# Optimization experiments

Hardware: AMD Instinct MI355X
Metric: run time of the kernel (lower is better)

## Reference

```python
import jax, jax.numpy as jnp
import numpy as np

HEADS = 16
ROPE_BASE = 10000.0


def _rope(x, cos, sin):
    # x: [B, H, L, hd]; rotate_half = [-x2, x1]
    x1, x2 = jnp.split(x, 2, axis=-1)
    rot = jnp.concatenate((-x2, x1), axis=-1)
    return x * cos + rot * sin


def setup_inputs() -> dict:
    key = jax.random.key(0)
    ks = jax.random.split(key, 8)
    B, L, D = 2, 2048, 1024
    s = 0.02
    inp = {
        "Q": jax.random.normal(ks[0], (B, L, D), jnp.float32),
        "K": jax.random.normal(ks[1], (B, L, D), jnp.float32),
        "V": jax.random.normal(ks[2], (B, L, D), jnp.float32),
        # Linear weights stored as [in, out] (transpose of torch's [out, in])
        "Wq": jax.random.normal(ks[3], (D, D), jnp.float32) * s,
        "Wk": jax.random.normal(ks[4], (D, D), jnp.float32) * s,
        "Wv": jax.random.normal(ks[5], (D, D), jnp.float32) * s,
        "Wo": jax.random.normal(ks[6], (D, D), jnp.float32) * s,
        "bq": jnp.zeros((D,), jnp.float32),
        "bk": jnp.zeros((D,), jnp.float32),
        "bv": jnp.zeros((D,), jnp.float32),
        "bo": jnp.zeros((D,), jnp.float32),
        # causal mask, 0 = masked, broadcast to [B,1,L,L]
        "mask": jnp.broadcast_to(jnp.tril(jnp.ones((L, L), jnp.int32))[None, None], (B, 1, L, L)),
    }
    return inp


def reference(Q, K, V, Wq, Wk, Wv, Wo, bq, bk, bv, bo, mask):
    B, L, D = Q.shape
    H = HEADS
    hd = D // H

    def proj(x, W, b):
        # [B,L,D] -> [B,H,L,hd]
        return (x @ W + b).reshape(B, -1, H, hd).transpose(0, 2, 1, 3)

    q = proj(Q, Wq, bq)
    k = proj(K, Wk, bk)
    v = proj(V, Wv, bv)

    # RoPE tables (deterministic constants)
    inv_freq = 1.0 / (ROPE_BASE ** (jnp.arange(0, hd, 2, dtype=jnp.float32) / hd))
    t = jnp.arange(L, dtype=jnp.float32)
    freqs = jnp.outer(t, inv_freq)              # [L, hd/2]
    emb = jnp.concatenate((freqs, freqs), -1)   # [L, hd]
    cos = jnp.cos(emb)[None, None]              # [1,1,L,hd]
    sin = jnp.sin(emb)[None, None]
    q = _rope(q, cos, sin)
    k = _rope(k, cos, sin)

    scale = jnp.sqrt(jnp.asarray(hd, q.dtype))
    scores = jnp.einsum('bhqd,bhkd->bhqk', q, k) / scale
    scores = jnp.where(mask == 0, jnp.asarray(-1e9, scores.dtype), scores)
    attn = jax.nn.softmax(scores, axis=-1)
    out = jnp.einsum('bhqk,bhkd->bhqd', attn, v)
    out = out.transpose(0, 2, 1, 3).reshape(B, L, D)
    return out @ Wo + bo
```

## Files before the change

kernel.cpp:

```cpp
#include <hip/hip_runtime.h>

typedef __attribute__((ext_vector_type(8))) short short8;
typedef __attribute__((ext_vector_type(4))) float f32x4;
typedef unsigned short u16;
typedef unsigned int u32;

#define MFMA_BF16(a, b, c) __builtin_amdgcn_mfma_f32_16x16x32_bf16((a), (b), (c), 0, 0, 0)

constexpr int D = 1024;
constexpr int L = 2048;
constexpr int NHEAD = 16;
constexpr int HD = 64;
constexpr float QLAMBDA = 0.125f * 1.44269504088896340736f;

__device__ __forceinline__ u16 f2bf(float f) {
  unsigned u = __builtin_bit_cast(unsigned, f);
  u = (u + 0x7fffu + ((u >> 16) & 1u)) >> 16;
  return (u16)u;
}

__device__ __forceinline__ short8 cvt8(f32x4 lo, f32x4 hi) {
  short8 r;
  r[0] = (short)f2bf(lo[0]); r[1] = (short)f2bf(lo[1]);
  r[2] = (short)f2bf(lo[2]); r[3] = (short)f2bf(lo[3]);
  r[4] = (short)f2bf(hi[0]); r[5] = (short)f2bf(hi[1]);
  r[6] = (short)f2bf(hi[2]); r[7] = (short)f2bf(hi[3]);
  return r;
}

__device__ __forceinline__ void gload16(const u16* src, u16* dst) {
  __builtin_amdgcn_global_load_lds(
      (const __attribute__((address_space(1))) u32*)(src),
      (__attribute__((address_space(3))) u32*)(dst), 16, 0, 0);
}

__global__ __launch_bounds__(256) void wt_trans_kernel(const float* W0, const float* W1,
                                                       const float* W2, const float* W3,
                                                       u16* out) {
  const float* W = blockIdx.z == 0 ? W0 : blockIdx.z == 1 ? W1 : blockIdx.z == 2 ? W2 : W3;
  u16* o = out + (size_t)blockIdx.z * D * D;
  __shared__ float t[32][33];
  int x = threadIdx.x & 31, y = threadIdx.x >> 5;
  int k0 = blockIdx.x * 32, n0 = blockIdx.y * 32;
#pragma unroll
  for (int i = 0; i < 4; i++) {
    int ky = y * 4 + i;
    t[ky][x] = W[(size_t)(k0 + ky) * D + n0 + x];
  }
  __syncthreads();
#pragma unroll
  for (int i = 0; i < 4; i++) {
    int ny = y * 4 + i;
    o[(size_t)(n0 + ny) * D + k0 + x] = f2bf(t[x][ny]);
  }
}

__global__ __launch_bounds__(256) void rope_tab_kernel(float* ct, float* st) {
  int t = blockIdx.x * 256 + threadIdx.x;
  int i = t & 31, pos = t >> 5;
  float invf = powf(10000.0f, -(float)i / 32.0f);
  float ang = (float)pos * invf;
  ct[t] = cosf(ang);
  st[t] = sinf(ang);
}

__global__ __launch_bounds__(256) void cvt_x_kernel(const float* Q, const float* K,
                                                    const float* V, u16* xb) {
  const float* src = blockIdx.y == 0 ? Q : blockIdx.y == 1 ? K : V;
  u16* dst = xb + (size_t)blockIdx.y * 4096 * D;
  int t = blockIdx.x * 256 + threadIdx.x;
  const float* p = src + (size_t)t * 8;
  f32x4 lo = *(const f32x4*)p;
  f32x4 hi = *(const f32x4*)(p + 4);
  *(short8*)(dst + (size_t)t * 8) = cvt8(lo, hi);
}


__global__ __launch_bounds__(256, 3) void proj_gemm_staged(
    const u16* xb, const u16* wT,
    const float* bq, const float* bk, const float* bv,
    const float* ct, const float* st,
    u16* qo, u16* ko, u16* vT) {
  int i = blockIdx.x;
  int swz = (i & 7) * 96 + (i >> 3);
  int z = swz >> 8;
  int bx = swz & 7;
  int by = (swz >> 3) & 31;

  const u16* A = xb + (size_t)z * 4096 * D;
  const u16* W = wT + (size_t)z * D * D;
  const float* bias = z == 0 ? bq : z == 1 ? bk : bv;

  int w = threadIdx.x >> 6, lane = threadIdx.x & 63;
  int r = lane & 15, c = lane >> 4;
  int wr = w >> 1, wc = w & 1;
  int m0 = by * 128 + wr * 64;
  int n0 = bx * 128 + wc * 64;

  __shared__ __align__(16) u16 lsA[2][4096];
  __shared__ __align__(16) u16 lsB[2][4096];

  const u16* aSrc[2];
  const u16* bSrc[2];
  int dstOff[2];
#pragma unroll
  for (int i2 = 0; i2 < 2; i2++) {
    int q0 = i2 * 256 + w * 64;
    int qq = q0 + lane;
    int t = qq >> 2;
    int gch = (qq & 3) ^ ((t >> 1) & 3);
    aSrc[i2] = A + (size_t)(by * 128 + t) * D + gch * 8;
    bSrc[i2] = W + (size_t)(bx * 128 + t) * D + gch * 8;
    dstOff[i2] = q0 * 8;
  }

  int aOff[4], bOff[4];
#pragma unroll
  for (int mi = 0; mi < 4; mi++) {
    int rowA = wr * 64 + mi * 16 + r;
    aOff[mi] = rowA * 32 + ((c ^ ((rowA >> 1) & 3)) << 3);
    int rowB = wc * 64 + mi * 16 + r;
    bOff[mi] = rowB * 32 + ((c ^ ((rowB >> 1) & 3)) << 3);
  }

  f32x4 acc[4][4];
#pragma unroll
  for (int mi = 0; mi < 4; mi++)
#pragma unroll
    for (int ni = 0; ni < 4; ni++) acc[mi][ni] = f32x4{0.f, 0.f, 0.f, 0.f};

#pragma unroll
  for (int i2 = 0; i2 < 2; i2++) {
    gload16(aSrc[i2], &lsA[0][dstOff[i2]]);
    gload16(bSrc[i2], &lsB[0][dstOff[i2]]);
  }

  auto compute = [&](const u16* pa, const u16* pb) {
    short8 af[4], bf[4];
#pragma unroll
    for (int mi = 0; mi < 4; mi++) af[mi] = *(const short8*)(pa + aOff[mi]);
#pragma unroll
    for (int ni = 0; ni < 4; ni++) bf[ni] = *(const short8*)(pb + bOff[ni]);
#pragma unroll
    for (int mi = 0; mi < 4; mi++)
#pragma unroll
      for (int ni = 0; ni < 4; ni++)
        acc[mi][ni] = MFMA_BF16(af[mi], bf[ni], acc[mi][ni]);
  };

  for (int kt = 0; kt < 31; kt++) {
    int cur = kt & 1;
    __syncthreads();
#pragma unroll
    for (int i2 = 0; i2 < 2; i2++) {
      gload16(aSrc[i2] + (kt + 1) * 32, &lsA[cur ^ 1][dstOff[i2]]);
      gload16(bSrc[i2] + (kt + 1) * 32, &lsB[cur ^ 1][dstOff[i2]]);
    }
    compute(lsA[cur], lsB[cur]);
  }
  __syncthreads();
  compute(lsA[1], lsB[1]);

  int h = n0 >> 6;
#pragma unroll
  for (int mi = 0; mi < 4; mi++) {
#pragma unroll
    for (int j = 0; j < 4; j++) {
      int grow = m0 + mi * 16 + c * 4 + j;
      int b = grow >> 11, ll = grow & 2047;
      if (z < 2) {
        u16* o = (z == 0) ? qo : ko;
        float lam = (z == 0) ? QLAMBDA : 1.0f;
        size_t dst = ((size_t)(b * NHEAD + h) * L + ll) * HD;
#pragma unroll
        for (int ni = 0; ni < 2; ni++) {
          int d = ni * 16 + r;
          float x1 = acc[mi][ni][j] + bias[n0 + d];
          float x2 = acc[mi][ni + 2][j] + bias[n0 + 32 + d];
          float cs = ct[ll * 32 + d], sn = st[ll * 32 + d];
          o[dst + d]      = f2bf((x1 * cs - x2 * sn) * lam);
          o[dst + d + 32] = f2bf((x2 * cs + x1 * sn) * lam);
        }
      } else {
#pragma unroll
        for (int ni = 0; ni < 4; ni++) {
          int d = ni * 16 + r;
          float val = acc[mi][ni][j] + bias[n0 + d];
          vT[((size_t)(b * NHEAD + h) * HD + d) * L + ll] = f2bf(val);
        }
      }
    }
  }
}

__global__ __launch_bounds__(256) void proj_gemm_f32(
    const float* Qf, const float* Kf, const float* Vf, const u16* wT,
    const float* bq, const float* bk, const float* bv,
    const float* ct, const float* st,
    u16* qo, u16* ko, u16* vT) {
  int i = blockIdx.x;
  int swz = (i & 7) * 96 + (i >> 3);
  int z = swz >> 8;
  int bx = swz & 7;
  int by = (swz >> 3) & 31;

  const u16* W = wT + (size_t)z * D * D;
  const float* bias = z == 0 ? bq : z == 1 ? bk : bv;

  int w = threadIdx.x >> 6, lane = threadIdx.x & 63;
  int r = lane & 15, c = lane >> 4;
  int wr = w >> 1, wc = w & 1;
  int m0 = by * 128 + wr * 64;
  int n0 = bx * 128 + wc * 64;

  const float* Af = z == 0 ? Qf : z == 1 ? Kf : Vf;
  const float* a0f = Af + (size_t)(m0 + r) * D + c * 8;
  const u16* b0 = W + (size_t)(n0 + r) * D + c * 8;

  f32x4 acc[4][4];
#pragma unroll
  for (int mi = 0; mi < 4; mi++)
#pragma unroll
    for (int ni = 0; ni < 4; ni++) acc[mi][ni] = f32x4{0.f, 0.f, 0.f, 0.f};

  for (int kk = 0; kk < D; kk += 32) {
    short8 af[4], bf[4];
#pragma unroll
    for (int mi = 0; mi < 4; mi++) {
      const float* ap = a0f + (size_t)mi * 16 * D;
      af[mi] = cvt8(*(const f32x4*)ap, *(const f32x4*)(ap + 4));
    }
#pragma unroll
    for (int ni = 0; ni < 4; ni++) bf[ni] = *(const short8*)(b0 + (size_t)ni * 16 * D);
#pragma unroll
    for (int mi = 0; mi < 4; mi++)
#pragma unroll
      for (int ni = 0; ni < 4; ni++)
        acc[mi][ni] = MFMA_BF16(af[mi], bf[ni], acc[mi][ni]);
    a0f += 32;
    b0 += 32;
  }

  int h = n0 >> 6;
#pragma unroll
  for (int mi = 0; mi < 4; mi++) {
#pragma unroll
    for (int j = 0; j < 4; j++) {
      int grow = m0 + mi * 16 + c * 4 + j;
      int b = grow >> 11, ll = grow & 2047;
      if (z < 2) {
        u16* o = (z == 0) ? qo : ko;
        float lam = (z == 0) ? QLAMBDA : 1.0f;
        size_t dst = ((size_t)(b * NHEAD + h) * L + ll) * HD;
#pragma unroll
        for (int ni = 0; ni < 2; ni++) {
          int d = ni * 16 + r;
          float x1 = acc[mi][ni][j] + bias[n0 + d];
          float x2 = acc[mi][ni + 2][j] + bias[n0 + 32 + d];
          float cs = ct[ll * 32 + d], sn = st[ll * 32 + d];
          o[dst + d]      = f2bf((x1 * cs - x2 * sn) * lam);
          o[dst + d + 32] = f2bf((x2 * cs + x1 * sn) * lam);
        }
      } else {
#pragma unroll
        for (int ni = 0; ni < 4; ni++) {
          int d = ni * 16 + r;
          float val = acc[mi][ni][j] + bias[n0 + d];
          vT[((size_t)(b * NHEAD + h) * HD + d) * L + ll] = f2bf(val);
        }
      }
    }
  }
}

__global__ __launch_bounds__(256) void attn_kernel(const u16* qg, const u16* kg,
                                                   const u16* vg, u16* O) {
  int i = blockIdx.x;
  int xcd = i & 7, j = i >> 3;
  int bh = xcd * 4 + (j & 3);
  int a = j >> 2;
  int qtA = a, qtB = 31 - a;

  int w = threadIdx.x >> 6, lane = threadIdx.x & 63;
  int r = lane & 15, c = lane >> 4;
  int qbA = qtA * 64 + w * 16;
  int qbB = qtB * 64 + w * 16;

  const u16* qp = qg + (size_t)bh * L * HD;
  const u16* kp = kg + (size_t)bh * L * HD;
  const u16* vp = vg + (size_t)bh * HD * L;

  __shared__ __align__(16) u16 kls[2][4096];
  __shared__ __align__(16) u16 vls[2][4096];
  __shared__ __align__(16) u16 plds[4][16][64];

  short8 aqA0 = *(const short8*)(qp + (size_t)(qbA + r) * HD + c * 8);
  short8 aqA1 = *(const short8*)(qp + (size_t)(qbA + r) * HD + 32 + c * 8);
  short8 aqB0 = *(const short8*)(qp + (size_t)(qbB + r) * HD + c * 8);
  short8 aqB1 = *(const short8*)(qp + (size_t)(qbB + r) * HD + 32 + c * 8);

  const short one_bf = (short)0x3F80;
  short8 ones = {one_bf, one_bf, one_bf, one_bf, one_bf, one_bf, one_bf, one_bf};

  f32x4 oA[4], oB[4];
  f32x4 sacA = f32x4{0.f, 0.f, 0.f, 0.f};
  f32x4 sacB = f32x4{0.f, 0.f, 0.f, 0.f};
#pragma unroll
  for (int n = 0; n < 4; n++) {
    oA[n] = f32x4{0.f, 0.f, 0.f, 0.f};
    oB[n] = f32x4{0.f, 0.f, 0.f, 0.f};
  }

  int nkt = qtB + 1;

#pragma unroll
  for (int rd = 0; rd < 2; rd++) {
    int q0 = (rd * 4 + w) << 6;
    int qq = q0 + lane;
    int row = qq >> 3;
    int gch = (qq & 7) ^ (row & 7);
    gload16(kp + (size_t)row * HD + gch * 8, &kls[0][q0 * 8]);
    gload16(vp + (size_t)row * L + gch * 8, &vls[0][q0 * 8]);
  }

  for (int kt = 0; kt < nkt; kt++) {
    int cur = kt & 1;
    __syncthreads();
    if (kt + 1 < nkt) {
      int kb2 = (kt + 1) * 64;
      const u16* kp2 = kp + (size_t)kb2 * HD;
      const u16* vp2 = vp + kb2;
#pragma unroll
      for (int rd = 0; rd < 2; rd++) {
        int q0 = (rd * 4 + w) << 6;
        int qq = q0 + lane;
        int row = qq >> 3;
        int gch = (qq & 7) ^ (row & 7);
        gload16(kp2 + (size_t)row * HD + gch * 8, &kls[cur ^ 1][q0 * 8]);
        gload16(vp2 + (size_t)row * L + gch * 8, &vls[cur ^ 1][q0 * 8]);
      }
    }
    const u16* kb_ = kls[cur];
    const u16* vb_ = vls[cur];
    int kbase = kt * 64;

    auto do_tile = [&](const short8& qf0, const short8& qf1, f32x4* o, f32x4& sac,
                       int qb, bool edge) {
      f32x4 S[4];
#pragma unroll
      for (int ks = 0; ks < 4; ks++) {
        int row = ks * 16 + r;
        short8 kf0 = *(const short8*)(kb_ + row * 64 + ((c ^ (row & 7)) << 3));
        short8 kf1 = *(const short8*)(kb_ + row * 64 + (((4 + c) ^ (row & 7)) << 3));
        S[ks] = f32x4{0.f, 0.f, 0.f, 0.f};
        S[ks] = MFMA_BF16(qf0, kf0, S[ks]);
        S[ks] = MFMA_BF16(qf1, kf1, S[ks]);
      }
#pragma unroll
      for (int j4 = 0; j4 < 4; j4++) {
        float p0 = exp2f(S[0][j4]);
        float p1 = exp2f(S[1][j4]);
        float p2 = exp2f(S[2][j4]);
        float p3 = exp2f(S[3][j4]);
        if (edge) {
          int qrow = qb + c * 4 + j4;
          if (kbase + r > qrow) p0 = 0.f;
          if (kbase + 16 + r > qrow) p1 = 0.f;
          if (kbase + 32 + r > qrow) p2 = 0.f;
          if (kbase + 48 + r > qrow) p3 = 0.f;
        }
        int prow = c * 4 + j4, xr = (prow & 7) << 3;
        plds[w][prow][(r) ^ xr]      = f2bf(p0);
        plds[w][prow][(16 + r) ^ xr] = f2bf(p1);
        plds[w][prow][(32 + r) ^ xr] = f2bf(p2);
        plds[w][prow][(48 + r) ^ xr] = f2bf(p3);
      }
      int xrr = (r & 7) << 3;
      short8 pa0 = *(const short8*)&plds[w][r][(c * 8) ^ xrr];
      short8 pa1 = *(const short8*)&plds[w][r][(32 + c * 8) ^ xrr];
      sac = MFMA_BF16(pa0, ones, sac);
      sac = MFMA_BF16(pa1, ones, sac);
#pragma unroll
      for (int n = 0; n < 4; n++) {
        int row = n * 16 + r;
        short8 vf0 = *(const short8*)(vb_ + row * 64 + ((c ^ (row & 7)) << 3));
        short8 vf1 = *(const short8*)(vb_ + row * 64 + (((4 + c) ^ (row & 7)) << 3));
        o[n] = MFMA_BF16(pa0, vf0, o[n]);
        o[n] = MFMA_BF16(pa1, vf1, o[n]);
      }
    };

    do_tile(aqB0, aqB1, oB, sacB, qbB, kt == nkt - 1);
    if (kt <= qtA) do_tile(aqA0, aqA1, oA, sacA, qbA, kt == qtA);
  }

  int b = bh >> 4, h = bh & 15;
#pragma unroll
  for (int j4 = 0; j4 < 4; j4++) {
    int qrowA = qbA + c * 4 + j4;
    int qrowB = qbB + c * 4 + j4;
    float invA = 1.0f / sacA[j4];
    float invB = 1.0f / sacB[j4];
#pragma unroll
    for (int n = 0; n < 4; n++) {
      O[((size_t)(b * L + qrowA)) * D + h * HD + n * 16 + r] = f2bf(oA[n][j4] * invA);
      O[((size_t)(b * L + qrowB)) * D + h * HD + n * 16 + r] = f2bf(oB[n][j4] * invB);
    }
  }
}

__global__ __launch_bounds__(256, 3) void oproj_gemm_staged(const u16* Ag, const u16* wT,
                                                            const float* bias, float* out) {
  int i = blockIdx.x;
  int swz = (i & 7) * 32 + (i >> 3);
  int bx = swz & 7, by = swz >> 3;

  int w = threadIdx.x >> 6, lane = threadIdx.x & 63;
  int r = lane & 15, c = lane >> 4;
  int wr = w >> 1, wc = w & 1;
  int m0 = by * 128 + wr * 64;
  int n0 = bx * 128 + wc * 64;

  __shared__ __align__(16) u16 lsA[2][4096];
  __shared__ __align__(16) u16 lsB[2][4096];

  const u16* aSrc[2];
  const u16* bSrc[2];
  int dstOff[2];
#pragma unroll
  for (int i2 = 0; i2 < 2; i2++) {
    int q0 = i2 * 256 + w * 64;
    int qq = q0 + lane;
    int t = qq >> 2;
    int gch = (qq & 3) ^ ((t >> 1) & 3);
    aSrc[i2] = Ag + (size_t)(by * 128 + t) * D + gch * 8;
    bSrc[i2] = wT + (size_t)(bx * 128 + t) * D + gch * 8;
    dstOff[i2] = q0 * 8;
  }

  int aOff[4], bOff[4];
#pragma unroll
  for (int mi = 0; mi < 4; mi++) {
    int rowA = wr * 64 + mi * 16 + r;
    aOff[mi] = rowA * 32 + ((c ^ ((rowA >> 1) & 3)) << 3);
    int rowB = wc * 64 + mi * 16 + r;
    bOff[mi] = rowB * 32 + ((c ^ ((rowB >> 1) & 3)) << 3);
  }

  f32x4 acc[4][4];
#pragma unroll
  for (int mi = 0; mi < 4; mi++)
#pragma unroll
    for (int ni = 0; ni < 4; ni++) acc[mi][ni] = f32x4{0.f, 0.f, 0.f, 0.f};

#pragma unroll
  for (int i2 = 0; i2 < 2; i2++) {
    gload16(aSrc[i2], &lsA[0][dstOff[i2]]);
    gload16(bSrc[i2], &lsB[0][dstOff[i2]]);
  }

  auto compute = [&](const u16* pa, const u16* pb) {
    short8 af[4], bf[4];
#pragma unroll
    for (int mi = 0; mi < 4; mi++) af[mi] = *(const short8*)(pa + aOff[mi]);
#pragma unroll
    for (int ni = 0; ni < 4; ni++) bf[ni] = *(const short8*)(pb + bOff[ni]);
#pragma unroll
    for (int mi = 0; mi < 4; mi++)
#pragma unroll
      for (int ni = 0; ni < 4; ni++)
        acc[mi][ni] = MFMA_BF16(af[mi], bf[ni], acc[mi][ni]);
  };

  for (int kt = 0; kt < 31; kt++) {
    int cur = kt & 1;
    __syncthreads();
#pragma unroll
    for (int i2 = 0; i2 < 2; i2++) {
      gload16(aSrc[i2] + (kt + 1) * 32, &lsA[cur ^ 1][dstOff[i2]]);
      gload16(bSrc[i2] + (kt + 1) * 32, &lsB[cur ^ 1][dstOff[i2]]);
    }
    compute(lsA[cur], lsB[cur]);
  }
  __syncthreads();
  compute(lsA[1], lsB[1]);

#pragma unroll
  for (int mi = 0; mi < 4; mi++)
#pragma unroll
    for (int j = 0; j < 4; j++) {
      int grow = m0 + mi * 16 + c * 4 + j;
#pragma unroll
      for (int ni = 0; ni < 4; ni++) {
        int gcol = n0 + ni * 16 + r;
        out[(size_t)grow * D + gcol] = acc[mi][ni][j] + bias[gcol];
      }
    }
}

extern "C" void kernel_launch(void* const* d_in, const int* in_sizes, int n_in,
                              void* d_out, int out_size, void* d_ws, size_t ws_size,
                              hipStream_t stream) {
  const float* Q = (const float*)d_in[0];
  const float* K = (const float*)d_in[1];
  const float* V = (const float*)d_in[2];
  const float* Wq = (const float*)d_in[3];
  const float* Wk = (const float*)d_in[4];
  const float* Wv = (const float*)d_in[5];
  const float* Wo = (const float*)d_in[6];
  const float* bq = (const float*)d_in[7];
  const float* bk = (const float*)d_in[8];
  const float* bv = (const float*)d_in[9];
  const float* bo = (const float*)d_in[10];
  float* out = (float*)d_out;

  char* ws = (char*)d_ws;
  u16* wT = (u16*)(ws);
  u16* woT = wT + (size_t)3 * 1024 * 1024;
  float* ct = (float*)(ws + 8388608);
  float* st = (float*)(ws + 8650752);
  u16* qbuf = (u16*)(ws + 8912896);
  u16* kbuf = (u16*)(ws + 17301504);
  u16* vbuf = (u16*)(ws + 25690112);
  u16* obuf = (u16*)(ws + 34078720);
  u16* xb = (u16*)(ws + 42467328);

  wt_trans_kernel<<<dim3(32, 32, 4), 256, 0, stream>>>(Wq, Wk, Wv, Wo, wT);
  rope_tab_kernel<<<dim3(256), 256, 0, stream>>>(ct, st);

  if (ws_size >= (size_t)67633152) {
    cvt_x_kernel<<<dim3(2048, 3), 256, 0, stream>>>(Q, K, V, xb);
    proj_gemm_staged<<<dim3(768), 256, 0, stream>>>(xb, wT, bq, bk, bv, ct, st,
                                                    qbuf, kbuf, vbuf);
  } else {
    proj_gemm_f32<<<dim3(768), 256, 0, stream>>>(Q, K, V, wT, bq, bk, bv, ct, st,
                                                 qbuf, kbuf, vbuf);
  }
  attn_kernel<<<dim3(512), 256, 0, stream>>>(qbuf, kbuf, vbuf, obuf);
  oproj_gemm_staged<<<dim3(256), 256, 0, stream>>>(obuf, woT, bo, out);
}
```

Baseline: 264.9 us.

## Merge prep kernels, use hardware bf16 convert, halve oproj tile height

Folds the weight transpose, RoPE table and input conversion kernels into one launch so fewer kernels are dispatched. Replaces the software round-to-nearest bf16 conversion with the hardware v_cvt_pk_bf16_f32 instruction in the projection epilogues and the attention kernel. Shrinks the output-projection tile from 128x128 to 64x128 and doubles its grid to 512 blocks, which spreads the work over more CUs but loads more weight data per output.

```diff
diff --git a/kernel.cpp b/kernel.cpp
--- a/kernel.cpp
+++ b/kernel.cpp
@@ -17,6 +17,12 @@
   unsigned u = __builtin_bit_cast(unsigned, f);
   u = (u + 0x7fffu + ((u >> 16) & 1u)) >> 16;
   return (u16)u;
+}
+
+__device__ __forceinline__ u16 cvt1(float f) {
+  unsigned o;
+  asm("v_cvt_pk_bf16_f32 %0, %1, %1" : "=v"(o) : "v"(f));
+  return (u16)o;
 }
 
 __device__ __forceinline__ short8 cvt8(f32x4 lo, f32x4 hi) {
@@ -34,45 +40,48 @@
       (__attribute__((address_space(3))) u32*)(dst), 16, 0, 0);
 }
 
-__global__ __launch_bounds__(256) void wt_trans_kernel(const float* W0, const float* W1,
-                                                       const float* W2, const float* W3,
-                                                       u16* out) {
-  const float* W = blockIdx.z == 0 ? W0 : blockIdx.z == 1 ? W1 : blockIdx.z == 2 ? W2 : W3;
-  u16* o = out + (size_t)blockIdx.z * D * D;
-  __shared__ float t[32][33];
-  int x = threadIdx.x & 31, y = threadIdx.x >> 5;
-  int k0 = blockIdx.x * 32, n0 = blockIdx.y * 32;
-#pragma unroll
-  for (int i = 0; i < 4; i++) {
-    int ky = y * 4 + i;
-    t[ky][x] = W[(size_t)(k0 + ky) * D + n0 + x];
-  }
-  __syncthreads();
-#pragma unroll
-  for (int i = 0; i < 4; i++) {
-    int ny = y * 4 + i;
-    o[(size_t)(n0 + ny) * D + k0 + x] = f2bf(t[x][ny]);
-  }
-}
-
-__global__ __launch_bounds__(256) void rope_tab_kernel(float* ct, float* st) {
-  int t = blockIdx.x * 256 + threadIdx.x;
-  int i = t & 31, pos = t >> 5;
-  float invf = powf(10000.0f, -(float)i / 32.0f);
-  float ang = (float)pos * invf;
-  ct[t] = cosf(ang);
-  st[t] = sinf(ang);
-}
-
-__global__ __launch_bounds__(256) void cvt_x_kernel(const float* Q, const float* K,
-                                                    const float* V, u16* xb) {
-  const float* src = blockIdx.y == 0 ? Q : blockIdx.y == 1 ? K : V;
-  u16* dst = xb + (size_t)blockIdx.y * 4096 * D;
-  int t = blockIdx.x * 256 + threadIdx.x;
-  const float* p = src + (size_t)t * 8;
-  f32x4 lo = *(const f32x4*)p;
-  f32x4 hi = *(const f32x4*)(p + 4);
-  *(short8*)(dst + (size_t)t * 8) = cvt8(lo, hi);
+template <bool DO_CVT>
+__global__ __launch_bounds__(256) void prep_kernel(
+    const float* W0, const float* W1, const float* W2, const float* W3, u16* wTout,
+    float* ct, float* st,
+    const float* Q, const float* K, const float* V, u16* xb) {
+  int i = blockIdx.x;
+  if (i < 4096) {
+    int z = i >> 10, bx = i & 31, by = (i >> 5) & 31;
+    const float* W = z == 0 ? W0 : z == 1 ? W1 : z == 2 ? W2 : W3;
+    u16* o = wTout + (size_t)z * D * D;
+    __shared__ float t[32][33];
+    int x = threadIdx.x & 31, y = threadIdx.x >> 5;
+    int k0 = bx * 32, n0 = by * 32;
+#pragma unroll
+    for (int q = 0; q < 4; q++) {
+      int ky = y * 4 + q;
+      t[ky][x] = W[(size_t)(k0 + ky) * D + n0 + x];
+    }
+    __syncthreads();
+#pragma unroll
+    for (int q = 0; q < 4; q++) {
+      int ny = y * 4 + q;
+      o[(size_t)(n0 + ny) * D + k0 + x] = f2bf(t[x][ny]);
+    }
+  } else if (i < 4352) {
+    int t = (i - 4096) * 256 + threadIdx.x;
+    int ii = t & 31, pos = t >> 5;
+    float invf = powf(10000.0f, -(float)ii / 32.0f);
+    float ang = (float)pos * invf;
+    ct[t] = cosf(ang);
+    st[t] = sinf(ang);
+  } else if constexpr (DO_CVT) {
+    int j = i - 4352;
+    int zz = j / 2048, bx = j - zz * 2048;
+    const float* src = zz == 0 ? Q : zz == 1 ? K : V;
+    u16* dst = xb + (size_t)zz * 4096 * D;
+    int t = bx * 256 + threadIdx.x;
+    const float* p = src + (size_t)t * 8;
+    f32x4 lo = *(const f32x4*)p;
+    f32x4 hi = *(const f32x4*)(p + 4);
+    *(short8*)(dst + (size_t)t * 8) = cvt8(lo, hi);
+  }
 }
 
 
@@ -178,15 +187,15 @@
           float x1 = acc[mi][ni][j] + bias[n0 + d];
           float x2 = acc[mi][ni + 2][j] + bias[n0 + 32 + d];
           float cs = ct[ll * 32 + d], sn = st[ll * 32 + d];
-          o[dst + d]      = f2bf((x1 * cs - x2 * sn) * lam);
-          o[dst + d + 32] = f2bf((x2 * cs + x1 * sn) * lam);
+          o[dst + d]      = cvt1((x1 * cs - x2 * sn) * lam);
+          o[dst + d + 32] = cvt1((x2 * cs + x1 * sn) * lam);
         }
       } else {
 #pragma unroll
         for (int ni = 0; ni < 4; ni++) {
           int d = ni * 16 + r;
           float val = acc[mi][ni][j] + bias[n0 + d];
-          vT[((size_t)(b * NHEAD + h) * HD + d) * L + ll] = f2bf(val);
+          vT[((size_t)(b * NHEAD + h) * HD + d) * L + ll] = cvt1(val);
         }
       }
     }
@@ -258,15 +267,15 @@
           float x1 = acc[mi][ni][j] + bias[n0 + d];
           float x2 = acc[mi][ni + 2][j] + bias[n0 + 32 + d];
           float cs = ct[ll * 32 + d], sn = st[ll * 32 + d];
-          o[dst + d]      = f2bf((x1 * cs - x2 * sn) * lam);
-          o[dst + d + 32] = f2bf((x2 * cs + x1 * sn) * lam);
+          o[dst + d]      = cvt1((x1 * cs - x2 * sn) * lam);
+          o[dst + d + 32] = cvt1((x2 * cs + x1 * sn) * lam);
         }
       } else {
 #pragma unroll
         for (int ni = 0; ni < 4; ni++) {
           int d = ni * 16 + r;
           float val = acc[mi][ni][j] + bias[n0 + d];
-          vT[((size_t)(b * NHEAD + h) * HD + d) * L + ll] = f2bf(val);
+          vT[((size_t)(b * NHEAD + h) * HD + d) * L + ll] = cvt1(val);
         }
       }
     }
@@ -370,10 +379,10 @@
           if (kbase + 48 + r > qrow) p3 = 0.f;
         }
         int prow = c * 4 + j4, xr = (prow & 7) << 3;
-        plds[w][prow][(r) ^ xr]      = f2bf(p0);
-        plds[w][prow][(16 + r) ^ xr] = f2bf(p1);
-        plds[w][prow][(32 + r) ^ xr] = f2bf(p2);
-        plds[w][prow][(48 + r) ^ xr] = f2bf(p3);
+        plds[w][prow][(r) ^ xr]      = cvt1(p0);
+        plds[w][prow][(16 + r) ^ xr] = cvt1(p1);
+        plds[w][prow][(32 + r) ^ xr] = cvt1(p2);
+        plds[w][prow][(48 + r) ^ xr] = cvt1(p3);
       }
       int xrr = (r & 7) << 3;
       short8 pa0 = *(const short8*)&plds[w][r][(c * 8) ^ xrr];
@@ -403,70 +412,75 @@
     float invB = 1.0f / sacB[j4];
 #pragma unroll
     for (int n = 0; n < 4; n++) {
-      O[((size_t)(b * L + qrowA)) * D + h * HD + n * 16 + r] = f2bf(oA[n][j4] * invA);
-      O[((size_t)(b * L + qrowB)) * D + h * HD + n * 16 + r] = f2bf(oB[n][j4] * invB);
-    }
-  }
-}
-
-__global__ __launch_bounds__(256, 3) void oproj_gemm_staged(const u16* Ag, const u16* wT,
-                                                            const float* bias, float* out) {
+      O[((size_t)(b * L + qrowA)) * D + h * HD + n * 16 + r] = cvt1(oA[n][j4] * invA);
+      O[((size_t)(b * L + qrowB)) * D + h * HD + n * 16 + r] = cvt1(oB[n][j4] * invB);
+    }
+  }
+}
+
+__global__ __launch_bounds__(256) void oproj_gemm_staged(const u16* Ag, const u16* wT,
+                                                         const float* bias, float* out) {
   int i = blockIdx.x;
-  int swz = (i & 7) * 32 + (i >> 3);
+  int swz = (i & 7) * 64 + (i >> 3);
   int bx = swz & 7, by = swz >> 3;
 
   int w = threadIdx.x >> 6, lane = threadIdx.x & 63;
   int r = lane & 15, c = lane >> 4;
   int wr = w >> 1, wc = w & 1;
-  int m0 = by * 128 + wr * 64;
+  int m0 = by * 64 + wr * 32;
   int n0 = bx * 128 + wc * 64;
 
-  __shared__ __align__(16) u16 lsA[2][4096];
+  __shared__ __align__(16) u16 lsA[2][2048];
   __shared__ __align__(16) u16 lsB[2][4096];
 
-  const u16* aSrc[2];
+  int qqA = w * 64 + lane;
+  int tA = qqA >> 2;
+  int gchA = (qqA & 3) ^ ((tA >> 1) & 3);
+  const u16* aSrc = Ag + (size_t)(by * 64 + tA) * D + gchA * 8;
+  int aDst = (w * 64) * 8;
+
   const u16* bSrc[2];
-  int dstOff[2];
+  int bDst[2];
 #pragma unroll
   for (int i2 = 0; i2 < 2; i2++) {
     int q0 = i2 * 256 + w * 64;
     int qq = q0 + lane;
     int t = qq >> 2;
     int gch = (qq & 3) ^ ((t >> 1) & 3);
-    aSrc[i2] = Ag + (size_t)(by * 128 + t) * D + gch * 8;
     bSrc[i2] = wT + (size_t)(bx * 128 + t) * D + gch * 8;
-    dstOff[i2] = q0 * 8;
-  }
-
-  int aOff[4], bOff[4];
-#pragma unroll
-  for (int mi = 0; mi < 4; mi++) {
-    int rowA = wr * 64 + mi * 16 + r;
+    bDst[i2] = q0 * 8;
+  }
+
+  int aOff[2], bOff[4];
+#pragma unroll
+  for (int mi = 0; mi < 2; mi++) {
+    int rowA = wr * 32 + mi * 16 + r;
     aOff[mi] = rowA * 32 + ((c ^ ((rowA >> 1) & 3)) << 3);
-    int rowB = wc * 64 + mi * 16 + r;
-    bOff[mi] = rowB * 32 + ((c ^ ((rowB >> 1) & 3)) << 3);
-  }
-
-  f32x4 acc[4][4];
-#pragma unroll
-  for (int mi = 0; mi < 4; mi++)
+  }
+#pragma unroll
+  for (int ni = 0; ni < 4; ni++) {
+    int rowB = wc * 64 + ni * 16 + r;
+    bOff[ni] = rowB * 32 + ((c ^ ((rowB >> 1) & 3)) << 3);
+  }
+
+  f32x4 acc[2][4];
+#pragma unroll
+  for (int mi = 0; mi < 2; mi++)
 #pragma unroll
     for (int ni = 0; ni < 4; ni++) acc[mi][ni] = f32x4{0.f, 0.f, 0.f, 0.f};
 
-#pragma unroll
-  for (int i2 = 0; i2 < 2; i2++) {
-    gload16(aSrc[i2], &lsA[0][dstOff[i2]]);
-    gload16(bSrc[i2], &lsB[0][dstOff[i2]]);
-  }
+  gload16(aSrc, &lsA[0][aDst]);
+#pragma unroll
+  for (int i2 = 0; i2 < 2; i2++) gload16(bSrc[i2], &lsB[0][bDst[i2]]);
 
   auto compute = [&](const u16* pa, const u16* pb) {
-    short8 af[4], bf[4];
-#pragma unroll
-    for (int mi = 0; mi < 4; mi++) af[mi] = *(const short8*)(pa + aOff[mi]);
+    short8 af[2], bf[4];
+#pragma unroll
+    for (int mi = 0; mi < 2; mi++) af[mi] = *(const short8*)(pa + aOff[mi]);
 #pragma unroll
     for (int ni = 0; ni < 4; ni++) bf[ni] = *(const short8*)(pb + bOff[ni]);
 #pragma unroll
-    for (int mi = 0; mi < 4; mi++)
+    for (int mi = 0; mi < 2; mi++)
 #pragma unroll
       for (int ni = 0; ni < 4; ni++)
         acc[mi][ni] = MFMA_BF16(af[mi], bf[ni], acc[mi][ni]);
@@ -475,18 +489,17 @@
   for (int kt = 0; kt < 31; kt++) {
     int cur = kt & 1;
     __syncthreads();
-#pragma unroll
-    for (int i2 = 0; i2 < 2; i2++) {
-      gload16(aSrc[i2] + (kt + 1) * 32, &lsA[cur ^ 1][dstOff[i2]]);
-      gload16(bSrc[i2] + (kt + 1) * 32, &lsB[cur ^ 1][dstOff[i2]]);
-    }
+    gload16(aSrc + (kt + 1) * 32, &lsA[cur ^ 1][aDst]);
+#pragma unroll
+    for (int i2 = 0; i2 < 2; i2++)
+      gload16(bSrc[i2] + (kt + 1) * 32, &lsB[cur ^ 1][bDst[i2]]);
     compute(lsA[cur], lsB[cur]);
   }
   __syncthreads();
   compute(lsA[1], lsB[1]);
 
 #pragma unroll
-  for (int mi = 0; mi < 4; mi++)
+  for (int mi = 0; mi < 2; mi++)
 #pragma unroll
     for (int j = 0; j < 4; j++) {
       int grow = m0 + mi * 16 + c * 4 + j;
@@ -525,17 +538,17 @@
   u16* obuf = (u16*)(ws + 34078720);
   u16* xb = (u16*)(ws + 42467328);
 
-  wt_trans_kernel<<<dim3(32, 32, 4), 256, 0, stream>>>(Wq, Wk, Wv, Wo, wT);
-  rope_tab_kernel<<<dim3(256), 256, 0, stream>>>(ct, st);
-
   if (ws_size >= (size_t)67633152) {
-    cvt_x_kernel<<<dim3(2048, 3), 256, 0, stream>>>(Q, K, V, xb);
+    prep_kernel<true><<<dim3(10496), 256, 0, stream>>>(Wq, Wk, Wv, Wo, wT, ct, st,
+                                                       Q, K, V, xb);
     proj_gemm_staged<<<dim3(768), 256, 0, stream>>>(xb, wT, bq, bk, bv, ct, st,
                                                     qbuf, kbuf, vbuf);
   } else {
+    prep_kernel<false><<<dim3(4352), 256, 0, stream>>>(Wq, Wk, Wv, Wo, wT, ct, st,
+                                                       Q, K, V, xb);
     proj_gemm_f32<<<dim3(768), 256, 0, stream>>>(Q, K, V, wT, bq, bk, bv, ct, st,
                                                  qbuf, kbuf, vbuf);
   }
   attn_kernel<<<dim3(512), 256, 0, stream>>>(qbuf, kbuf, vbuf, obuf);
-  oproj_gemm_staged<<<dim3(256), 256, 0, stream>>>(obuf, woT, bo, out);
-}
+  oproj_gemm_staged<<<dim3(512), 256, 0, stream>>>(obuf, woT, bo, out);
+}
```

Result: faster. 256.0 us (-3.4%).
